# Optimization experiments

Hardware: AMD Instinct MI355X
Metric: run time of the kernel (lower is better)

## Reference

```python
import jax, jax.numpy as jnp
import numpy as np

N_NODES = 100000
N_EDGES = 3200000
IN_DIM = 512
HIDDEN = 256
NUM_CLASSES = 1000


def setup_inputs() -> dict:
    key = jax.random.key(0)
    ks = jax.random.split(key, 9)
    x = jax.random.normal(ks[0], (N_NODES, IN_DIM), dtype=jnp.float32)
    edge_index = jax.random.randint(ks[1], (2, N_EDGES), 0, N_NODES, dtype=jnp.int64)
    # GCNConv params (PyG: weight [in, out], bias [out])
    W1 = jax.random.normal(ks[2], (IN_DIM, HIDDEN), dtype=jnp.float32) / np.sqrt(IN_DIM)
    b1 = jnp.zeros((HIDDEN,), dtype=jnp.float32)
    W2 = jax.random.normal(ks[3], (HIDDEN, HIDDEN), dtype=jnp.float32) / np.sqrt(HIDDEN)
    b2 = jnp.zeros((HIDDEN,), dtype=jnp.float32)
    Wfc = jax.random.normal(ks[4], (HIDDEN, NUM_CLASSES), dtype=jnp.float32) / np.sqrt(HIDDEN)
    bfc = jnp.zeros((NUM_CLASSES,), dtype=jnp.float32)
    return {"x": x, "edge_index": edge_index, "W1": W1, "b1": b1,
            "W2": W2, "b2": b2, "Wfc": Wfc, "bfc": bfc}


def _gcn_norm(edge_index, num_nodes):
    # add self loops, compute sym-normalized edge weights (PyG GCNConv default)
    loop = jnp.arange(num_nodes, dtype=edge_index.dtype)
    row = jnp.concatenate([edge_index[0], loop])  # source
    col = jnp.concatenate([edge_index[1], loop])  # target
    ones = jnp.ones(row.shape[0], dtype=jnp.float32)
    deg = jax.ops.segment_sum(ones, col, num_segments=num_nodes)
    dinv = jnp.where(deg > 0, jax.lax.rsqrt(deg), 0.0)
    norm = dinv[row] * dinv[col]
    return row, col, norm


def _gcn_conv(x, W, b, row, col, norm, num_nodes):
    h = x @ W                                     # [N, out]
    msg = h[row] * norm[:, None]                  # gather + scale
    agg = jax.ops.segment_sum(msg, col, num_segments=num_nodes)
    return agg + b


def reference(x, edge_index, W1, b1, W2, b2, Wfc, bfc):
    n = x.shape[0]
    row, col, norm = _gcn_norm(edge_index, n)
    h = jax.nn.relu(_gcn_conv(x, W1, b1, row, col, norm, n))
    h = jax.nn.relu(_gcn_conv(h, W2, b2, row, col, norm, n))
    return h @ Wfc + bfc
```

## Files before the change

### kernel.cpp

```cpp
#include <hip/hip_runtime.h>
#include <hip/hip_bf16.h>
#include <cstdint>
#include <cstddef>

#define N_NODES 100000
#define N_EDGES 3200000
#define IN_DIM 512
#define HIDDEN 256
#define NUM_CLASSES 1000
#define SCAN_CHUNK 1024


__device__ __forceinline__ float bf2f(unsigned short u) {
  union { unsigned int i; float f; } c; c.i = ((unsigned int)u) << 16; return c.f;
}
__device__ __forceinline__ unsigned short f2bf(float f) {
  union { float f; unsigned int i; } c; c.f = f;
  unsigned int i = c.i;
  unsigned int r = i + 0x7FFFu + ((i >> 16) & 1u);
  return (unsigned short)(r >> 16);
}

typedef __attribute__((ext_vector_type(8))) short bf16x8;
typedef __attribute__((ext_vector_type(4))) float f32x4;


__global__ void k_zero_cnt(int* __restrict__ cnt, int n) {
  int i = blockIdx.x * blockDim.x + threadIdx.x;
  if (i < n) cnt[i] = 0;
}

__global__ void k_hist(const int* __restrict__ col, int* __restrict__ cnt, int e) {
  int i = blockIdx.x * blockDim.x + threadIdx.x;
  if (i < e) atomicAdd(&cnt[col[i]], 1);
}

__global__ void k_scan_block_sums(const int* __restrict__ cnt, int* __restrict__ blk, int n) {
  __shared__ int s[256];
  int t = threadIdx.x;
  int base = blockIdx.x * SCAN_CHUNK + t * 4;
  int sum = 0;
#pragma unroll
  for (int k = 0; k < 4; ++k) { int i = base + k; if (i < n) sum += cnt[i]; }
  s[t] = sum; __syncthreads();
  for (int off = 128; off > 0; off >>= 1) {
    if (t < off) s[t] += s[t + off];
    __syncthreads();
  }
  if (t == 0) blk[blockIdx.x] = s[0];
}

__global__ void k_scan_tops(int* __restrict__ blk, int nb, int* __restrict__ total) {
  __shared__ int s[128];
  int t = threadIdx.x;
  int v = (t < nb) ? blk[t] : 0;
  s[t] = v; __syncthreads();
  for (int off = 1; off < 128; off <<= 1) {
    int x = (t >= off) ? s[t - off] : 0;
    __syncthreads();
    s[t] += x;
    __syncthreads();
  }
  if (t < nb) blk[t] = s[t] - v;
  if (t == 0) *total = s[127];
}

__global__ void k_scan_final(const int* __restrict__ cnt, const int* __restrict__ blk,
                             int* __restrict__ csr_off, int* __restrict__ cursor,
                             float* __restrict__ dinv, int n) {
  __shared__ int s[256];
  int t = threadIdx.x;
  int base = blockIdx.x * SCAN_CHUNK + t * 4;
  int v[4]; int sum = 0;
#pragma unroll
  for (int k = 0; k < 4; ++k) { int i = base + k; v[k] = (i < n) ? cnt[i] : 0; sum += v[k]; }
  s[t] = sum; __syncthreads();
  for (int off = 1; off < 256; off <<= 1) {
    int x = (t >= off) ? s[t - off] : 0;
    __syncthreads();
    s[t] += x;
    __syncthreads();
  }
  int run = blk[blockIdx.x] + ((t == 0) ? 0 : s[t - 1]);
#pragma unroll
  for (int k = 0; k < 4; ++k) {
    int i = base + k;
    if (i < n) {
      csr_off[i] = run;
      cursor[i] = run;
      dinv[i] = rsqrtf((float)(v[k] + 1));
    }
    run += v[k];
  }
}

__global__ void k_fill(const int* __restrict__ row, const int* __restrict__ col,
                       int* __restrict__ cursor, int* __restrict__ csr_row, int e) {
  int i = blockIdx.x * blockDim.x + threadIdx.x;
  if (i < e) {
    int c = col[i];
    int slot = atomicAdd(&cursor[c], 1);
    csr_row[slot] = row[i];
  }
}


__global__ void k_split_x(const float4* __restrict__ x, ushort4* __restrict__ xh,
                          ushort4* __restrict__ xl, int n4) {
  int i = blockIdx.x * blockDim.x + threadIdx.x;
  int stride = gridDim.x * blockDim.x;
  for (; i < n4; i += stride) {
    float4 v = x[i];
    ushort4 h, l;
    h.x = f2bf(v.x); l.x = f2bf(v.x - bf2f(h.x));
    h.y = f2bf(v.y); l.y = f2bf(v.y - bf2f(h.y));
    h.z = f2bf(v.z); l.z = f2bf(v.z - bf2f(h.z));
    h.w = f2bf(v.w); l.w = f2bf(v.w - bf2f(h.w));
    xh[i] = h; xl[i] = l;
  }
}


__global__ void k_prep_w(const float* __restrict__ W, int K, int N, int Npad,
                         unsigned short* __restrict__ hi, unsigned short* __restrict__ lo,
                         unsigned short* __restrict__ hi2) {
  int idx = blockIdx.x * blockDim.x + threadIdx.x;
  int total = (K >> 3) * Npad;
  if (idx >= total) return;
  int kb = idx / Npad, n = idx - kb * Npad;
  unsigned short h8[8], l8[8];
#pragma unroll
  for (int j = 0; j < 8; ++j) {
    float v = (n < N) ? W[(size_t)(kb * 8 + j) * N + n] : 0.f;
    unsigned short h = f2bf(v);
    float r = v - bf2f(h);
    h8[j] = h; l8[j] = f2bf(r);
  }
  size_t off = (size_t)idx * 8;
#pragma unroll
  for (int j = 0; j < 8; ++j) { hi[off + j] = h8[j]; lo[off + j] = l8[j]; }
  if (hi2) {
#pragma unroll
    for (int j = 0; j < 8; ++j) hi2[off + j] = h8[j];
  }
}


template <bool C_BF16, bool ROW_SCALE, bool ADD_BIAS>
__global__ __launch_bounds__(256, 2) void k_mfma_gemm(
    const unsigned short* __restrict__ A0,
    const unsigned short* __restrict__ A1,
    const unsigned short* __restrict__ A2,
    const unsigned short* __restrict__ Bp,
    const float* __restrict__ rowscale,
    const float* __restrict__ bias,
    void* __restrict__ Cv,
    int M, int N, int Npad, int Kseg, int nseg) {
  __shared__ __align__(16) unsigned short As[1024 * 8];
  __shared__ __align__(16) unsigned short Bs[1024 * 8];
  const int tid = threadIdx.x;
  const int wid = tid >> 6, lane = tid & 63;
  const int lr = lane & 15, lk = lane >> 4;
  const int m0 = blockIdx.y * 128, n0 = blockIdx.x * 128;
  const int m0w = (wid >> 1) * 64, n0w = (wid & 1) * 64;

  f32x4 acc[4][4] = {};

  const int KTOT = Kseg * nseg;
  int seg = 0, kin = 0;
  for (int kt = 0; kt < KTOT; kt += 64) {
    const unsigned short* Aseg = (seg == 0) ? A0 : ((seg == 1) ? A1 : A2);
#pragma unroll
    for (int r = 0; r < 4; ++r) {
      int c = r * 256 + tid;
      int kbl = c >> 7, m = c & 127;
      int gm = m0 + m; if (gm > M - 1) gm = M - 1;
      const unsigned short* src = Aseg + (size_t)gm * Kseg + (kin + kbl * 8);
      unsigned short* dst = &As[(size_t)(r * 256 + (wid << 6)) * 8];
      __builtin_amdgcn_global_load_lds(
          (const __attribute__((address_space(1))) unsigned int*)src,
          (__attribute__((address_space(3))) unsigned int*)dst, 16, 0, 0);
    }
    const int kb0 = kt >> 3;
#pragma unroll
    for (int r = 0; r < 4; ++r) {
      int c = r * 256 + tid;
      int kbl = c >> 7, n = c & 127;
      const unsigned short* src = Bp + ((size_t)(kb0 + kbl) * Npad + (n0 + n)) * 8;
      unsigned short* dst = &Bs[(size_t)(r * 256 + (wid << 6)) * 8];
      __builtin_amdgcn_global_load_lds(
          (const __attribute__((address_space(1))) unsigned int*)src,
          (__attribute__((address_space(3))) unsigned int*)dst, 16, 0, 0);
    }
    __syncthreads();
#pragma unroll
    for (int kh = 0; kh < 2; ++kh) {
      bf16x8 bfr[4];
#pragma unroll
      for (int nf = 0; nf < 4; ++nf)
        bfr[nf] = *(const bf16x8*)&Bs[(size_t)((((kh * 4 + lk) << 7) + n0w + nf * 16 + lr)) * 8];
#pragma unroll
      for (int mf = 0; mf < 4; ++mf) {
        bf16x8 af = *(const bf16x8*)&As[(size_t)((((kh * 4 + lk) << 7) + m0w + mf * 16 + lr)) * 8];
#pragma unroll
        for (int nf = 0; nf < 4; ++nf)
          acc[mf][nf] = __builtin_amdgcn_mfma_f32_16x16x32_bf16(af, bfr[nf], acc[mf][nf], 0, 0, 0);
      }
    }
    __syncthreads();
    kin += 64;
    if (kin == Kseg) { kin = 0; ++seg; }
  }

  const int orow = lk * 4;
#pragma unroll
  for (int mf = 0; mf < 4; ++mf) {
#pragma unroll
    for (int i = 0; i < 4; ++i) {
      int gm = m0 + m0w + mf * 16 + orow + i;
      if (gm >= M) continue;
      float rs = ROW_SCALE ? rowscale[gm] : 1.0f;
#pragma unroll
      for (int nf = 0; nf < 4; ++nf) {
        int gn = n0 + n0w + nf * 16 + lr;
        if (gn >= N) continue;
        float o = acc[mf][nf][i] * rs;
        if (ADD_BIAS) o += bias[gn];
        if constexpr (C_BF16) {
          ((unsigned short*)Cv)[(size_t)gm * N + gn] = f2bf(o);
        } else {
          ((float*)Cv)[(size_t)gm * N + gn] = o;
        }
      }
    }
  }
}


__global__ __launch_bounds__(256) void k_agg_bias_relu(
    const ushort4* __restrict__ Hs, const int* __restrict__ csr_off,
    const int* __restrict__ csr_row, const float* __restrict__ dinv,
    const float* __restrict__ bias, ushort4* __restrict__ out, int n) {
  int node = blockIdx.x * 4 + (threadIdx.x >> 6);
  if (node >= n) return;
  int lane = threadIdx.x & 63;
  ushort4 sv = Hs[(size_t)node * 64 + lane];
  float ax = bf2f(sv.x), ay = bf2f(sv.y), az = bf2f(sv.z), aw = bf2f(sv.w);
  int beg = csr_off[node], end = csr_off[node + 1];
  for (int j = beg; j < end; ++j) {
    int r = csr_row[j];
    ushort4 v = Hs[(size_t)r * 64 + lane];
    ax += bf2f(v.x); ay += bf2f(v.y); az += bf2f(v.z); aw += bf2f(v.w);
  }
  float di = dinv[node];
  float4 b = ((const float4*)bias)[lane];
  ushort4 o;
  o.x = f2bf(fmaxf(fmaf(ax, di, b.x), 0.f));
  o.y = f2bf(fmaxf(fmaf(ay, di, b.y), 0.f));
  o.z = f2bf(fmaxf(fmaf(az, di, b.z), 0.f));
  o.w = f2bf(fmaxf(fmaf(aw, di, b.w), 0.f));
  out[(size_t)node * 64 + lane] = o;
}


extern "C" void kernel_launch(void* const* d_in, const int* in_sizes, int n_in,
                              void* d_out, int out_size, void* d_ws, size_t ws_size,
                              hipStream_t stream) {
  const float* x   = (const float*)d_in[0];
  const int*   ei  = (const int*)d_in[1];
  const float* W1  = (const float*)d_in[2];
  const float* b1  = (const float*)d_in[3];
  const float* W2  = (const float*)d_in[4];
  const float* b2  = (const float*)d_in[5];
  const float* Wfc = (const float*)d_in[6];
  const float* bfc = (const float*)d_in[7];
  float* out = (float*)d_out;

  const int* row = ei;
  const int* col = ei + N_EDGES;

  char* q = (char*)d_out;
  unsigned short* bufA    = (unsigned short*)q;
  int*            csr_row = (int*)(q + 51200000);
  unsigned short* Xh      = (unsigned short*)(q + 64000000);
  unsigned short* Xl      = (unsigned short*)(q + 166400000);
  unsigned short* Bp1     = (unsigned short*)(q + 268800000);
  unsigned short* Bp2     = (unsigned short*)(q + 269600000);

  char* p = (char*)d_ws;
  auto alloc = [&](size_t bytes) { char* r = p; p += (bytes + 255) & ~(size_t)255; return r; };
  int*   cnt     = (int*)alloc(sizeof(int) * N_NODES);
  int*   csr_off = (int*)alloc(sizeof(int) * (N_NODES + 1));
  int*   cursor  = (int*)alloc(sizeof(int) * N_NODES);
  int*   blk     = (int*)alloc(sizeof(int) * 128);
  float* dinv    = (float*)alloc(sizeof(float) * N_NODES);
  unsigned short* bufB = (unsigned short*)alloc(sizeof(unsigned short) * (size_t)N_NODES * HIDDEN);
  unsigned short* BpFC = (unsigned short*)alloc(sizeof(unsigned short) * (size_t)2 * 32 * 1024 * 8);

  const int nscan = (N_NODES + SCAN_CHUNK - 1) / SCAN_CHUNK;

  hipLaunchKernelGGL(k_split_x, dim3(2048), dim3(256), 0, stream,
                     (const float4*)x, (ushort4*)Xh, (ushort4*)Xl, N_NODES * IN_DIM / 4);
  hipLaunchKernelGGL(k_prep_w, dim3((64 * 256 + 255) / 256), dim3(256), 0, stream,
                     W1, IN_DIM, HIDDEN, HIDDEN, Bp1, Bp1 + (size_t)64 * 256 * 8,
                     Bp1 + (size_t)2 * 64 * 256 * 8);
  hipLaunchKernelGGL(k_prep_w, dim3((32 * 256 + 255) / 256), dim3(256), 0, stream,
                     W2, HIDDEN, HIDDEN, HIDDEN, Bp2, Bp2 + (size_t)32 * 256 * 8,
                     (unsigned short*)nullptr);
  hipLaunchKernelGGL(k_prep_w, dim3((32 * 1024 + 255) / 256), dim3(256), 0, stream,
                     Wfc, HIDDEN, NUM_CLASSES, 1024, BpFC, BpFC + (size_t)32 * 1024 * 8,
                     (unsigned short*)nullptr);

  hipLaunchKernelGGL(k_zero_cnt, dim3((N_NODES + 255) / 256), dim3(256), 0, stream, cnt, N_NODES);
  hipLaunchKernelGGL(k_hist, dim3((N_EDGES + 255) / 256), dim3(256), 0, stream, col, cnt, N_EDGES);
  hipLaunchKernelGGL(k_scan_block_sums, dim3(nscan), dim3(256), 0, stream, cnt, blk, N_NODES);
  hipLaunchKernelGGL(k_scan_tops, dim3(1), dim3(128), 0, stream, blk, nscan, csr_off + N_NODES);
  hipLaunchKernelGGL(k_scan_final, dim3(nscan), dim3(256), 0, stream, cnt, blk, csr_off, cursor, dinv, N_NODES);
  hipLaunchKernelGGL(k_fill, dim3((N_EDGES + 255) / 256), dim3(256), 0, stream, row, col, cursor, csr_row, N_EDGES);

  const int MB = (N_NODES + 127) / 128;

  hipLaunchKernelGGL((k_mfma_gemm<true, true, false>), dim3(HIDDEN / 128, MB), dim3(256), 0, stream,
                     Xh, Xh, Xl, Bp1, dinv, (const float*)nullptr, bufA,
                     N_NODES, HIDDEN, HIDDEN, IN_DIM, 3);
  hipLaunchKernelGGL(k_agg_bias_relu, dim3((N_NODES + 3) / 4), dim3(256), 0, stream,
                     (const ushort4*)bufA, csr_off, csr_row, dinv, b1, (ushort4*)bufB, N_NODES);

  hipLaunchKernelGGL((k_mfma_gemm<true, true, false>), dim3(HIDDEN / 128, MB), dim3(256), 0, stream,
                     bufB, bufB, bufB, Bp2, dinv, (const float*)nullptr, bufA,
                     N_NODES, HIDDEN, HIDDEN, HIDDEN, 2);
  hipLaunchKernelGGL(k_agg_bias_relu, dim3((N_NODES + 3) / 4), dim3(256), 0, stream,
                     (const ushort4*)bufA, csr_off, csr_row, dinv, b2, (ushort4*)bufB, N_NODES);

  hipLaunchKernelGGL((k_mfma_gemm<false, false, true>), dim3(1024 / 128, MB), dim3(256), 0, stream,
                     bufB, bufB, bufB, BpFC, (const float*)nullptr, bfc, out,
                     N_NODES, NUM_CLASSES, 1024, HIDDEN, 2);
}
```

Measured before the change: 2.057 ms.

## Reuse A tiles across split-precision B segments and batch neighbor gathers

The GEMM now loads each A tile once and multiplies it against all B segments that share it (for example the hi/lo weight splits), rather than reloading A for each segment. This halves A traffic for segments that use the same source. LDS for B doubles and launch bounds now ask for 3 blocks per CU, which may push register pressure. The aggregation kernel loads 64 CSR indices per wave at once, broadcasts them with shuffles, and issues 8 gathers before accumulating, to raise memory-level parallelism.

```diff
diff --git a/kernel.cpp b/kernel.cpp
--- a/kernel.cpp
+++ b/kernel.cpp
@@ -147,17 +147,16 @@
 
 
 template <bool C_BF16, bool ROW_SCALE, bool ADD_BIAS>
-__global__ __launch_bounds__(256, 2) void k_mfma_gemm(
-    const unsigned short* __restrict__ A0,
-    const unsigned short* __restrict__ A1,
-    const unsigned short* __restrict__ A2,
+__global__ __launch_bounds__(256, 3) void k_mfma_gemm(
+    const unsigned short* __restrict__ A0, int nb0,
+    const unsigned short* __restrict__ A1, int nb1,
     const unsigned short* __restrict__ Bp,
     const float* __restrict__ rowscale,
     const float* __restrict__ bias,
     void* __restrict__ Cv,
-    int M, int N, int Npad, int Kseg, int nseg) {
+    int M, int N, int Npad, int Kseg) {
   __shared__ __align__(16) unsigned short As[1024 * 8];
-  __shared__ __align__(16) unsigned short Bs[1024 * 8];
+  __shared__ __align__(16) unsigned short Bs[2048 * 8];
   const int tid = threadIdx.x;
   const int wid = tid >> 6, lane = tid & 63;
   const int lr = lane & 15, lk = lane >> 4;
@@ -165,51 +164,59 @@
   const int m0w = (wid >> 1) * 64, n0w = (wid & 1) * 64;
 
   f32x4 acc[4][4] = {};
-
-  const int KTOT = Kseg * nseg;
-  int seg = 0, kin = 0;
-  for (int kt = 0; kt < KTOT; kt += 64) {
-    const unsigned short* Aseg = (seg == 0) ? A0 : ((seg == 1) ? A1 : A2);
-#pragma unroll
-    for (int r = 0; r < 4; ++r) {
-      int c = r * 256 + tid;
-      int kbl = c >> 7, m = c & 127;
-      int gm = m0 + m; if (gm > M - 1) gm = M - 1;
-      const unsigned short* src = Aseg + (size_t)gm * Kseg + (kin + kbl * 8);
-      unsigned short* dst = &As[(size_t)(r * 256 + (wid << 6)) * 8];
-      __builtin_amdgcn_global_load_lds(
-          (const __attribute__((address_space(1))) unsigned int*)src,
-          (__attribute__((address_space(3))) unsigned int*)dst, 16, 0, 0);
-    }
-    const int kb0 = kt >> 3;
-#pragma unroll
-    for (int r = 0; r < 4; ++r) {
-      int c = r * 256 + tid;
-      int kbl = c >> 7, n = c & 127;
-      const unsigned short* src = Bp + ((size_t)(kb0 + kbl) * Npad + (n0 + n)) * 8;
-      unsigned short* dst = &Bs[(size_t)(r * 256 + (wid << 6)) * 8];
-      __builtin_amdgcn_global_load_lds(
-          (const __attribute__((address_space(1))) unsigned int*)src,
-          (__attribute__((address_space(3))) unsigned int*)dst, 16, 0, 0);
-    }
-    __syncthreads();
-#pragma unroll
-    for (int kh = 0; kh < 2; ++kh) {
-      bf16x8 bfr[4];
-#pragma unroll
-      for (int nf = 0; nf < 4; ++nf)
-        bfr[nf] = *(const bf16x8*)&Bs[(size_t)((((kh * 4 + lk) << 7) + n0w + nf * 16 + lr)) * 8];
-#pragma unroll
-      for (int mf = 0; mf < 4; ++mf) {
-        bf16x8 af = *(const bf16x8*)&As[(size_t)((((kh * 4 + lk) << 7) + m0w + mf * 16 + lr)) * 8];
-#pragma unroll
-        for (int nf = 0; nf < 4; ++nf)
-          acc[mf][nf] = __builtin_amdgcn_mfma_f32_16x16x32_bf16(af, bfr[nf], acc[mf][nf], 0, 0, 0);
-      }
-    }
-    __syncthreads();
-    kin += 64;
-    if (kin == Kseg) { kin = 0; ++seg; }
+  const int kbseg = Kseg >> 3;
+
+  int segbase = 0;
+  for (int src = 0; src < 2; ++src) {
+    const int nb = (src == 0) ? nb0 : nb1;
+    if (nb == 0) continue;
+    const unsigned short* A = (src == 0) ? A0 : A1;
+    for (int kt = 0; kt < Kseg; kt += 64) {
+#pragma unroll
+      for (int r = 0; r < 4; ++r) {
+        int c = r * 256 + tid;
+        int kbl = c >> 7, m = c & 127;
+        int gm = m0 + m; if (gm > M - 1) gm = M - 1;
+        const unsigned short* srcp = A + (size_t)gm * Kseg + (kt + kbl * 8);
+        unsigned short* dst = &As[(size_t)(r * 256 + (wid << 6)) * 8];
+        __builtin_amdgcn_global_load_lds(
+            (const __attribute__((address_space(1))) unsigned int*)srcp,
+            (__attribute__((address_space(3))) unsigned int*)dst, 16, 0, 0);
+      }
+      const int kb0 = kt >> 3;
+      for (int s = 0; s < nb; ++s) {
+#pragma unroll
+        for (int r = 0; r < 4; ++r) {
+          int c = r * 256 + tid;
+          int kbl = c >> 7, n = c & 127;
+          const unsigned short* srcp =
+              Bp + ((size_t)((segbase + s) * kbseg + kb0 + kbl) * Npad + (n0 + n)) * 8;
+          unsigned short* dst = &Bs[(size_t)(s * 1024 + r * 256 + (wid << 6)) * 8];
+          __builtin_amdgcn_global_load_lds(
+              (const __attribute__((address_space(1))) unsigned int*)srcp,
+              (__attribute__((address_space(3))) unsigned int*)dst, 16, 0, 0);
+        }
+      }
+      __syncthreads();
+      for (int s = 0; s < nb; ++s) {
+#pragma unroll
+        for (int kh = 0; kh < 2; ++kh) {
+          bf16x8 bfr[4];
+#pragma unroll
+          for (int nf = 0; nf < 4; ++nf)
+            bfr[nf] = *(const bf16x8*)&Bs[(size_t)(s * 1024 + (((kh * 4 + lk) << 7) + n0w + nf * 16 + lr)) * 8];
+#pragma unroll
+          for (int mf = 0; mf < 4; ++mf) {
+            bf16x8 af = *(const bf16x8*)&As[(size_t)((((kh * 4 + lk) << 7) + m0w + mf * 16 + lr)) * 8];
+#pragma unroll
+            for (int nf = 0; nf < 4; ++nf)
+              acc[mf][nf] = __builtin_amdgcn_mfma_f32_16x16x32_bf16(af, bfr[nf], acc[mf][nf], 0, 0, 0);
+          }
+        }
+      }
+      __syncthreads();
+    }
+    segbase += nb;
   }
 
   const int orow = lk * 4;
@@ -247,18 +254,36 @@
   ushort4 sv = Hs[(size_t)node * 64 + lane];
   float ax = bf2f(sv.x), ay = bf2f(sv.y), az = bf2f(sv.z), aw = bf2f(sv.w);
   int beg = csr_off[node], end = csr_off[node + 1];
-  for (int j = beg; j < end; ++j) {
-    int r = csr_row[j];
-    ushort4 v = Hs[(size_t)r * 64 + lane];
-    ax += bf2f(v.x); ay += bf2f(v.y); az += bf2f(v.z); aw += bf2f(v.w);
+  for (int b = beg; b < end; b += 64) {
+    int idx = (b + lane < end) ? csr_row[b + lane] : 0;
+    int cnt = min(end - b, 64);
+    int j = 0;
+    for (; j + 8 <= cnt; j += 8) {
+      ushort4 v[8];
+#pragma unroll
+      for (int u = 0; u < 8; ++u) {
+        int r = __shfl(idx, j + u);
+        v[u] = Hs[(size_t)r * 64 + lane];
+      }
+#pragma unroll
+      for (int u = 0; u < 8; ++u) {
+        ax += bf2f(v[u].x); ay += bf2f(v[u].y);
+        az += bf2f(v[u].z); aw += bf2f(v[u].w);
+      }
+    }
+    for (; j < cnt; ++j) {
+      int r = __shfl(idx, j);
+      ushort4 v = Hs[(size_t)r * 64 + lane];
+      ax += bf2f(v.x); ay += bf2f(v.y); az += bf2f(v.z); aw += bf2f(v.w);
+    }
   }
   float di = dinv[node];
-  float4 b = ((const float4*)bias)[lane];
+  float4 b4 = ((const float4*)bias)[lane];
   ushort4 o;
-  o.x = f2bf(fmaxf(fmaf(ax, di, b.x), 0.f));
-  o.y = f2bf(fmaxf(fmaf(ay, di, b.y), 0.f));
-  o.z = f2bf(fmaxf(fmaf(az, di, b.z), 0.f));
-  o.w = f2bf(fmaxf(fmaf(aw, di, b.w), 0.f));
+  o.x = f2bf(fmaxf(fmaf(ax, di, b4.x), 0.f));
+  o.y = f2bf(fmaxf(fmaf(ay, di, b4.y), 0.f));
+  o.z = f2bf(fmaxf(fmaf(az, di, b4.z), 0.f));
+  o.w = f2bf(fmaxf(fmaf(aw, di, b4.w), 0.f));
   out[(size_t)node * 64 + lane] = o;
 }
 
@@ -321,18 +346,18 @@
   const int MB = (N_NODES + 127) / 128;
 
   hipLaunchKernelGGL((k_mfma_gemm<true, true, false>), dim3(HIDDEN / 128, MB), dim3(256), 0, stream,
-                     Xh, Xh, Xl, Bp1, dinv, (const float*)nullptr, bufA,
-                     N_NODES, HIDDEN, HIDDEN, IN_DIM, 3);
+                     Xh, 2, Xl, 1, Bp1, dinv, (const float*)nullptr, bufA,
+                     N_NODES, HIDDEN, HIDDEN, IN_DIM);
   hipLaunchKernelGGL(k_agg_bias_relu, dim3((N_NODES + 3) / 4), dim3(256), 0, stream,
                      (const ushort4*)bufA, csr_off, csr_row, dinv, b1, (ushort4*)bufB, N_NODES);
 
   hipLaunchKernelGGL((k_mfma_gemm<true, true, false>), dim3(HIDDEN / 128, MB), dim3(256), 0, stream,
-                     bufB, bufB, bufB, Bp2, dinv, (const float*)nullptr, bufA,
-                     N_NODES, HIDDEN, HIDDEN, HIDDEN, 2);
+                     bufB, 2, (const unsigned short*)nullptr, 0, Bp2, dinv, (const float*)nullptr, bufA,
+                     N_NODES, HIDDEN, HIDDEN, HIDDEN);
   hipLaunchKernelGGL(k_agg_bias_relu, dim3((N_NODES + 3) / 4), dim3(256), 0, stream,
                      (const ushort4*)bufA, csr_off, csr_row, dinv, b2, (ushort4*)bufB, N_NODES);
 
   hipLaunchKernelGGL((k_mfma_gemm<false, false, true>), dim3(1024 / 128, MB), dim3(256), 0, stream,
-                     bufB, bufB, bufB, BpFC, (const float*)nullptr, bfc, out,
-                     N_NODES, NUM_CLASSES, 1024, HIDDEN, 2);
-}
+                     bufB, 2, (const unsigned short*)nullptr, 0, BpFC, (const float*)nullptr, bfc, out,
+                     N_NODES, NUM_CLASSES, 1024, HIDDEN);
+}
```

Result: faster. 1.783 ms (-13.3%).
